# Performance work log

Hardware: AMD Instinct MI355X
Metric: run time of the kernel (lower is better)

The kernel has to match this reference:

```python
import jax, jax.numpy as jnp
import numpy as np

RATIO = 0.08  # self.ratio_3 (frozen parameter)
# kernel point k -> (dx, dy) = (k//3-1, k%3-1); matches torch.meshgrid('ij') flattening in offset_modulation
GX = np.repeat(np.arange(-1, 2), 3)  # [-1,-1,-1,0,0,0,1,1,1]
GY = np.tile(np.arange(-1, 2), 3)    # [-1,0,1,-1,0,1,-1,0,1]


def conv3(x, w, b):
    y = jax.lax.conv_general_dilated(x, w, (1, 1), ((1, 1), (1, 1)),
                                     dimension_numbers=('NCHW', 'OIHW', 'NCHW'))
    return y + b[None, :, None, None]


def offset_modulation(offset):
    B, C, H, W = offset.shape
    ov = offset.reshape(B, C // 2, 2, H, W)
    crop = ov[:, 3:12]                      # 9 (x,y) pairs
    oxy = jnp.concatenate([crop[:, :, 0], crop[:, :, 1]], axis=1) * RATIO  # [B,18,H,W]
    grid = jnp.concatenate([jnp.asarray(GX), jnp.asarray(GY)]).astype(offset.dtype)
    return oxy - grid[None, :, None, None]


def bilinear_sample(x, py, px):
    # x: [B,C,H,W]; py,px: [B,H,W] float sample coords; zero outside bounds
    B, C, H, W = x.shape
    y0 = jnp.floor(py); x0 = jnp.floor(px)
    wy = py - y0; wx = px - x0
    def gather(yi, xi):
        valid = ((yi >= 0) & (yi < H) & (xi >= 0) & (xi < W)).astype(x.dtype)
        yc = jnp.clip(yi, 0, H - 1).astype(jnp.int32)
        xc = jnp.clip(xi, 0, W - 1).astype(jnp.int32)
        g = jax.vmap(lambda img, yy, xx: img[:, yy, xx])(x, yc, xc)  # [B,C,H,W]
        return g * valid[:, None]
    return (gather(y0, x0) * ((1 - wy) * (1 - wx))[:, None]
            + gather(y0, x0 + 1) * ((1 - wy) * wx)[:, None]
            + gather(y0 + 1, x0) * (wy * (1 - wx))[:, None]
            + gather(y0 + 1, x0 + 1) * (wy * wx)[:, None])


def deform_conv(x, off, w, b):
    # off: [B,18,H,W], channels 0..8 = dx per kernel point, 9..17 = dy
    B, C, H, W = x.shape
    by = jnp.arange(H, dtype=x.dtype)[None, :, None]
    bx = jnp.arange(W, dtype=x.dtype)[None, None, :]
    out = jnp.zeros((B, w.shape[0], H, W), x.dtype)
    for k in range(9):
        py = by + GY[k] + off[:, 9 + k]
        px = bx + GX[k] + off[:, k]
        s = bilinear_sample(x, py, px)
        out = out + jnp.einsum('bchw,oc->bohw', s, w[:, :, GY[k] + 1, GX[k] + 1])
    return out + b[None, :, None, None]


def setup_inputs():
    key = jax.random.key(0)
    ks = iter(jax.random.split(key, 32))
    def p(*shape):
        return jax.random.normal(next(ks), shape, jnp.float32) * 0.05
    inp = {
        'x': jax.random.normal(next(ks), (2, 64, 256, 256), jnp.float32),
        'offset_0': jax.random.normal(next(ks), (2, 24, 256, 256), jnp.float32),
        'l12_w': p(64, 64, 3, 3), 'l12_b': p(64),
        'l13_w1': p(64, 64, 3, 3), 'l13_b1': p(64),
        'l13_w2': p(64, 64, 3, 3), 'l13_b2': p(64),
        'l14_w1': p(64, 64, 3, 3), 'l14_b1': p(64),
        'l14_w2': p(64, 64, 3, 3), 'l14_b2': p(64),
        'l15_w': p(32, 64, 3, 3), 'l15_b': p(32),
        'd50_w': p(32, 32, 3, 3), 'd50_b': p(32),
        'd51_w': p(32, 32, 3, 3), 'd51_b': p(32),
        'd60_w': p(32, 32, 3, 3), 'd60_b': p(32),
        'd61_w': p(32, 32, 3, 3), 'd61_b': p(32),
        'l24_w': p(3, 32, 3, 3), 'l24_b': p(3),
    }
    return inp


def reference(x, offset_0, l12_w, l12_b, l13_w1, l13_b1, l13_w2, l13_b2,
              l14_w1, l14_b1, l14_w2, l14_b2, l15_w, l15_b,
              d50_w, d50_b, d51_w, d51_b, d60_w, d60_b, d61_w, d61_b,
              l24_w, l24_b):
    off = offset_modulation(offset_0)
    x = conv3(x, l12_w, l12_b)
    x = conv3(jax.nn.relu(conv3(x, l13_w1, l13_b1)), l13_w2, l13_b2) + x
    x = conv3(jax.nn.relu(conv3(x, l14_w1, l14_b1)), l14_w2, l14_b2) + x
    x = conv3(x, l15_w, l15_b)
    r5 = jax.nn.relu(deform_conv(x, off, d50_w, d50_b))
    r5 = deform_conv(r5, off, d51_w, d51_b)
    x = x + r5
    r6 = jax.nn.relu(deform_conv(x, off, d60_w, d60_b))
    r6 = deform_conv(r6, off, d61_w, d61_b)
    x = x + r6
    return conv3(x, l24_w, l24_b)
```

## Files before the change

### kernel.cpp

```cpp
#include <hip/hip_runtime.h>

#define HH 256
#define WW 256
#define HW (HH * WW)

typedef float f32x4 __attribute__((ext_vector_type(4)));
typedef float f32x2 __attribute__((ext_vector_type(2)));
typedef short bf16x8 __attribute__((ext_vector_type(8)));

__device__ __forceinline__ unsigned short f2bf(float f) {
    union { float f; unsigned u; } v; v.f = f;
    unsigned r = v.u + 0x7fff + ((v.u >> 16) & 1);
    return (unsigned short)(r >> 16);
}
__device__ __forceinline__ float bflo(unsigned u) {
    union { unsigned u; float f; } v; v.u = u << 16; return v.f;
}
__device__ __forceinline__ float bfhi(unsigned u) {
    union { unsigned u; float f; } v; v.u = u & 0xffff0000u; return v.f;
}
__device__ __forceinline__ unsigned cvtpk(float lo, float hi) {
    unsigned r;
    asm("v_cvt_pk_bf16_f32 %0, %1, %2" : "=v"(r) : "v"(lo), "v"(hi));
    return r;
}
__device__ __forceinline__ f32x2 pkmul(f32x2 a, f32x2 b) {
    f32x2 d;
    asm("v_pk_mul_f32 %0, %1, %2" : "=v"(d) : "v"(a), "v"(b));
    return d;
}
__device__ __forceinline__ f32x2 pkfma(f32x2 a, f32x2 b, f32x2 c) {
    f32x2 d;
    asm("v_pk_fma_f32 %0, %1, %2, %3" : "=v"(d) : "v"(a), "v"(b), "v"(c));
    return d;
}
__device__ __forceinline__ f32x2 up2(unsigned u) {
    f32x2 r;
    union { unsigned u; float f; } lo, hi;
    lo.u = u << 16; hi.u = u & 0xffff0000u;
    r[0] = lo.f; r[1] = hi.f;
    return r;
}

template <int W>
__device__ __forceinline__ bf16x8 lerp8(const unsigned short* __restrict__ tile,
                                        int lp, float wx, float wy, int kg) {
    const unsigned short* p = tile + lp * 40 + kg * 8;
    uint4 a00 = *(const uint4*)p;
    uint4 a01 = *(const uint4*)(p + 40);
    uint4 a10 = *(const uint4*)(p + W * 40);
    uint4 a11 = *(const uint4*)(p + W * 40 + 40);
    float omx = 1.f - wx, omy = 1.f - wy;
    float s00 = omy * omx, s01 = omy * wx, s10 = wy * omx, s11 = wy * wx;
    f32x2 w00p = {s00, s00}, w01p = {s01, s01}, w10p = {s10, s10}, w11p = {s11, s11};
    unsigned c00[4] = {a00.x, a00.y, a00.z, a00.w};
    unsigned c01[4] = {a01.x, a01.y, a01.z, a01.w};
    unsigned c10[4] = {a10.x, a10.y, a10.z, a10.w};
    unsigned c11[4] = {a11.x, a11.y, a11.z, a11.w};
    union { bf16x8 v; unsigned u[4]; } ur;
#pragma unroll
    for (int j = 0; j < 4; ++j) {
        f32x2 s = pkmul(w00p, up2(c00[j]));
        s = pkfma(w01p, up2(c01[j]), s);
        s = pkfma(w10p, up2(c10[j]), s);
        s = pkfma(w11p, up2(c11[j]), s);
        ur.u[j] = cvtpk(s[0], s[1]);
    }
    return ur.v;
}

__global__ void prepack_all(
    const float* w0, const float* w1, const float* w2, const float* w3,
    const float* w4, const float* w5, const float* w6, const float* w7,
    const float* w8, const float* w9,
    unsigned short* d0, unsigned short* d1, unsigned short* d2,
    unsigned short* d3, unsigned short* d4, unsigned short* d5,
    unsigned short* d6, unsigned short* d7, unsigned short* d8,
    unsigned short* d9) {
    const int L = blockIdx.y;
    const float* w; unsigned short* dst; int COUT, CIN;
    switch (L) {
        case 0: w = w0; dst = d0; COUT = 64; CIN = 64; break;
        case 1: w = w1; dst = d1; COUT = 64; CIN = 64; break;
        case 2: w = w2; dst = d2; COUT = 64; CIN = 64; break;
        case 3: w = w3; dst = d3; COUT = 64; CIN = 64; break;
        case 4: w = w4; dst = d4; COUT = 64; CIN = 64; break;
        case 5: w = w5; dst = d5; COUT = 32; CIN = 64; break;
        case 6: w = w6; dst = d6; COUT = 32; CIN = 32; break;
        case 7: w = w7; dst = d7; COUT = 32; CIN = 32; break;
        case 8: w = w8; dst = d8; COUT = 32; CIN = 32; break;
        default: w = w9; dst = d9; COUT = 32; CIN = 32; break;
    }
    int n = COUT * CIN * 9;
    int i = blockIdx.x * 256 + threadIdx.x;
    if (i >= n) return;
    int q = i & 31;
    int rest = i >> 5;
    int o = rest % COUT;
    int rest2 = rest / COUT;
    int KC = CIN >> 5;
    int kc = rest2 % KC;
    int t = rest2 / KC;
    int cin = kc * 32 + q;
    float v = w[((o * CIN + cin) * 3 + t / 3) * 3 + (t % 3)];
    dst[i] = f2bf(v);
}

template <bool SRCF32, int CIN, int COUT, bool RELU, bool ADDRES>
__global__ __launch_bounds__((COUT / 32) * 128) void convmfma(
    const void* __restrict__ in_, const unsigned short* __restrict__ wp,
    const float* __restrict__ bias, const unsigned short* __restrict__ res,
    unsigned short* __restrict__ out) {
    constexpr int KC = CIN / 32;
    constexpr int WM = COUT / 32;
    constexpr int NT = WM * 128;
    constexpr int CSTR = (CIN == 64) ? 72 : 40;
    __shared__ unsigned short xt[204 * CSTR];

    const int tid = threadIdx.x;
    const int b = blockIdx.z;
    const int bx0 = blockIdx.x * 32;
    const int by0 = blockIdx.y * 4;

    if (SRCF32) {
        const float* inb = (const float*)in_ + (size_t)b * CIN * HW;
        for (int hp = tid; hp < 204; hp += NT) {
            int hy = hp / 34, hx = hp - hy * 34;
            int gy = by0 + hy - 1, gx = bx0 + hx - 1;
            bool ok = ((unsigned)gy < HH) && ((unsigned)gx < WW);
            const float* src = inb + ((size_t)gy * WW + gx);
            unsigned* dstp = (unsigned*)&xt[hp * CSTR];
#pragma unroll 4
            for (int c = 0; c < CIN; c += 2) {
                float v0 = ok ? src[(size_t)c * HW] : 0.f;
                float v1 = ok ? src[(size_t)(c + 1) * HW] : 0.f;
                dstp[c >> 1] = cvtpk(v0, v1);
            }
        }
    } else {
        const unsigned short* inb = (const unsigned short*)in_ + (size_t)b * HW * CIN;
        constexpr int CH = CIN / 8;
        for (int idx = tid; idx < 204 * CH; idx += NT) {
            int hp = idx / CH, sub = idx - hp * CH;
            int hy = hp / 34, hx = hp - hy * 34;
            int gy = by0 + hy - 1, gx = bx0 + hx - 1;
            uint4 v = {0, 0, 0, 0};
            if (((unsigned)gy < HH) && ((unsigned)gx < WW))
                v = *(const uint4*)&inb[((size_t)gy * WW + gx) * CIN + sub * 8];
            *(uint4*)&xt[hp * CSTR + sub * 8] = v;
        }
    }
    __syncthreads();

    const int lane = tid & 63;
    const int wv = tid >> 6;
    const int wm = (WM == 2) ? (wv & 1) : 0;
    const int wn = (WM == 2) ? (wv >> 1) : wv;
    const int l15 = lane & 15;
    const int kg = lane >> 4;

    f32x4 acc[2][4];
#pragma unroll
    for (int m = 0; m < 2; ++m)
#pragma unroll
        for (int n = 0; n < 4; ++n) acc[m][n] = {0.f, 0.f, 0.f, 0.f};

    int hbase[4];
#pragma unroll
    for (int n = 0; n < 4; ++n) {
        int p = wn * 64 + n * 16 + l15;
        hbase[n] = (p >> 5) * 34 + (p & 31);
    }

    const unsigned short* wlane = wp + ((size_t)(wm * 32 + l15) * 4 + kg) * 8;

#pragma unroll
    for (int t = 0; t < 9; ++t) {
        bf16x8 afr[2][KC];
#pragma unroll
        for (int kc = 0; kc < KC; ++kc)
#pragma unroll
            for (int m = 0; m < 2; ++m)
                afr[m][kc] = *(const bf16x8*)(wlane + ((size_t)(t * KC + kc) * COUT + m * 16) * 32);

        const int hoff = (t / 3) * 34 + (t % 3);
#pragma unroll
        for (int kc = 0; kc < KC; ++kc) {
            bf16x8 bfr[4];
#pragma unroll
            for (int n = 0; n < 4; ++n)
                bfr[n] = *(const bf16x8*)&xt[(hbase[n] + hoff) * CSTR + kc * 32 + kg * 8];
#pragma unroll
            for (int m = 0; m < 2; ++m)
#pragma unroll
                for (int n = 0; n < 4; ++n)
                    acc[m][n] = __builtin_amdgcn_mfma_f32_16x16x32_bf16(afr[m][kc], bfr[n], acc[m][n], 0, 0, 0);
        }
    }

    const size_t pixbase = (size_t)b * HW;
#pragma unroll
    for (int m = 0; m < 2; ++m) {
#pragma unroll
        for (int n = 0; n < 4; ++n) {
            int p = wn * 64 + n * 16 + l15;
            int gy = by0 + (p >> 5), gx = bx0 + (p & 31);
            size_t pidx = (pixbase + (size_t)gy * WW + gx) * COUT;
            int cb = wm * 32 + m * 16 + kg * 4;
            float v[4];
#pragma unroll
            for (int r = 0; r < 4; ++r) {
                v[r] = acc[m][n][r] + bias[cb + r];
                if (RELU) v[r] = fmaxf(v[r], 0.f);
            }
            if (ADDRES) {
                uint2 rr = *(const uint2*)&res[pidx + cb];
                v[0] += bflo(rr.x); v[1] += bfhi(rr.x);
                v[2] += bflo(rr.y); v[3] += bfhi(rr.y);
            }
            uint2 o;
            o.x = cvtpk(v[0], v[1]);
            o.y = cvtpk(v[2], v[3]);
            *(uint2*)&out[pidx + cb] = o;
        }
    }
}

__global__ __launch_bounds__(512) void dpair(
    const unsigned short* __restrict__ in, const float* __restrict__ off0,
    const unsigned short* __restrict__ w1p, const float* __restrict__ b1,
    const unsigned short* __restrict__ w2p, const float* __restrict__ b2,
    unsigned short* __restrict__ out) {
    constexpr int CS = 40;
    __shared__ unsigned short xt[432 * CS];

    const int tid = threadIdx.x;
    const int b = blockIdx.z;
    const int bx0 = blockIdx.x * 32;
    const int by0 = blockIdx.y * 8;

    const unsigned short* inb = in + (size_t)b * HW * 32;
    for (int idx = tid; idx < 432 * 4; idx += 512) {
        int hp = idx >> 2, sub = idx & 3;
        int hy = hp / 36, hx = hp - hy * 36;
        int gy = by0 + hy - 2, gx = bx0 + hx - 2;
        uint4 v = {0, 0, 0, 0};
        if (((unsigned)gy < HH) && ((unsigned)gx < WW))
            v = *(const uint4*)&inb[((size_t)gy * WW + gx) * 32 + sub * 8];
        *(uint4*)&xt[hp * CS + sub * 8] = v;
    }
    __syncthreads();

    const int lane = tid & 63;
    const int wv = tid >> 6;
    const int l15 = lane & 15;
    const int kg = lane >> 4;
    const float* offB = off0 + (size_t)b * 24 * HW;

    f32x4 acc1[2][3];
#pragma unroll
    for (int m = 0; m < 2; ++m)
#pragma unroll
        for (int f = 0; f < 3; ++f) acc1[m][f] = {0.f, 0.f, 0.f, 0.f};

    int fgy[3], fgx[3], foff[3];
#pragma unroll
    for (int f = 0; f < 3; ++f) {
        int id = (wv * 3 + f) * 16 + l15;
        int rid = min(id, 339);
        int iy = rid / 34, ix = rid - iy * 34;
        fgy[f] = by0 - 1 + iy;
        fgx[f] = bx0 - 1 + ix;
        int cy = min(max(fgy[f], 0), HH - 1);
        int cx = min(max(fgx[f], 0), WW - 1);
        foff[f] = cy * WW + cx;
    }
    const unsigned short* w1l = w1p + (size_t)(l15 * 32 + kg * 8);

#pragma unroll 1
    for (int t = 0; t < 9; ++t) {
        const int k = (t % 3) * 3 + t / 3;
        const float* offx = offB + (size_t)(6 + 2 * k) * HW;
        const float* offy = offB + (size_t)(7 + 2 * k) * HW;
        bf16x8 afr[2];
#pragma unroll
        for (int m = 0; m < 2; ++m)
            afr[m] = *(const bf16x8*)(w1l + (size_t)(t * 32 + m * 16) * 32);

#pragma unroll
        for (int f = 0; f < 3; ++f) {
            if ((wv * 3 + f) * 16 >= 340) continue;
            float dxv = offx[foff[f]] * 0.08f;
            float dyv = offy[foff[f]] * 0.08f;
            float pxf = (float)fgx[f] + dxv;
            float pyf = (float)fgy[f] + dyv;
            float x0f = floorf(pxf), y0f = floorf(pyf);
            float wx = pxf - x0f, wy = pyf - y0f;
            int tx0 = min(max((int)x0f - (bx0 - 2), 0), 34);
            int ty0 = min(max((int)y0f - (by0 - 2), 0), 10);
            bf16x8 bfr = lerp8<36>(xt, ty0 * 36 + tx0, wx, wy, kg);
#pragma unroll
            for (int m = 0; m < 2; ++m)
                acc1[m][f] = __builtin_amdgcn_mfma_f32_16x16x32_bf16(afr[m], bfr, acc1[m][f], 0, 0, 0);
        }
    }
    __syncthreads();

#pragma unroll
    for (int f = 0; f < 3; ++f) {
        int id = (wv * 3 + f) * 16 + l15;
        bool ok = ((unsigned)fgy[f] < HH) && ((unsigned)fgx[f] < WW) && (id < 340);
        int wid = min(id, 351);
#pragma unroll
        for (int m = 0; m < 2; ++m) {
            int cb = m * 16 + kg * 4;
            float v[4];
#pragma unroll
            for (int r = 0; r < 4; ++r)
                v[r] = ok ? fmaxf(acc1[m][f][r] + b1[cb + r], 0.f) : 0.f;
            uint2 o;
            o.x = cvtpk(v[0], v[1]);
            o.y = cvtpk(v[2], v[3]);
            *(uint2*)&xt[wid * CS + cb] = o;
        }
    }
    __syncthreads();

    f32x4 acc2[2][2];
#pragma unroll
    for (int m = 0; m < 2; ++m)
#pragma unroll
        for (int n = 0; n < 2; ++n) acc2[m][n] = {0.f, 0.f, 0.f, 0.f};

    const int py = by0 + wv;
    const unsigned short* w2l = w2p + (size_t)(l15 * 32 + kg * 8);

#pragma unroll 1
    for (int t = 0; t < 9; ++t) {
        const int k = (t % 3) * 3 + t / 3;
        const float* offx = offB + (size_t)(6 + 2 * k) * HW + (size_t)py * WW;
        const float* offy = offB + (size_t)(7 + 2 * k) * HW + (size_t)py * WW;
        bf16x8 afr[2];
#pragma unroll
        for (int m = 0; m < 2; ++m)
            afr[m] = *(const bf16x8*)(w2l + (size_t)(t * 32 + m * 16) * 32);

        bf16x8 bfr[2];
#pragma unroll
        for (int n = 0; n < 2; ++n) {
            const int pxi = bx0 + n * 16 + l15;
            float dxv = offx[pxi] * 0.08f;
            float dyv = offy[pxi] * 0.08f;
            float pxf = (float)pxi + dxv;
            float pyf = (float)py + dyv;
            float x0f = floorf(pxf), y0f = floorf(pyf);
            float wx = pxf - x0f, wy = pyf - y0f;
            int mx0 = min(max((int)x0f - (bx0 - 1), 0), 32);
            int my0 = min(max((int)y0f - (by0 - 1), 0), 8);
            bfr[n] = lerp8<34>(xt, my0 * 34 + mx0, wx, wy, kg);
        }
#pragma unroll
        for (int m = 0; m < 2; ++m)
#pragma unroll
            for (int n = 0; n < 2; ++n)
                acc2[m][n] = __builtin_amdgcn_mfma_f32_16x16x32_bf16(afr[m], bfr[n], acc2[m][n], 0, 0, 0);
    }

    unsigned short* outb = out + (size_t)b * HW * 32;
#pragma unroll
    for (int n = 0; n < 2; ++n) {
        int gx = bx0 + n * 16 + l15;
        size_t pidx = ((size_t)py * WW + gx) * 32;
#pragma unroll
        for (int m = 0; m < 2; ++m) {
            int cb = m * 16 + kg * 4;
            float v[4];
#pragma unroll
            for (int r = 0; r < 4; ++r) v[r] = acc2[m][n][r] + b2[cb + r];
            uint2 rr = *(const uint2*)&inb[pidx + cb];
            v[0] += bflo(rr.x); v[1] += bfhi(rr.x);
            v[2] += bflo(rr.y); v[3] += bfhi(rr.y);
            uint2 o;
            o.x = cvtpk(v[0], v[1]);
            o.y = cvtpk(v[2], v[3]);
            *(uint2*)&outb[pidx + cb] = o;
        }
    }
}

__global__ __launch_bounds__(256) void conv3f(const unsigned short* __restrict__ in,
                                              const float* __restrict__ wgt,
                                              const float* __restrict__ bias,
                                              float* __restrict__ out) {
    __shared__ unsigned short xt[324 * 34];
    const int tid = threadIdx.x;
    const int lx = tid & 15, ly = tid >> 4;
    const int bx = blockIdx.x << 4, by = blockIdx.y << 4;
    const int b = blockIdx.z;

    const unsigned short* inb = in + (size_t)b * HW * 32;
    for (int idx = tid; idx < 324 * 8; idx += 256) {
        int hp = idx >> 3, sub = idx & 7;
        int hy = hp / 18, hx = hp - hy * 18;
        int gy = by + hy - 1, gx = bx + hx - 1;
        uint2 v = {0, 0};
        if (((unsigned)gy < HH) && ((unsigned)gx < WW))
            v = *(const uint2*)&inb[((size_t)gy * WW + gx) * 32 + sub * 4];
        *(uint2*)&xt[hp * 34 + sub * 4] = v;
    }
    __syncthreads();

    float a0 = bias[0], a1 = bias[1], a2 = bias[2];
#pragma unroll
    for (int ty = 0; ty < 3; ++ty) {
#pragma unroll
        for (int tx = 0; tx < 3; ++tx) {
            const unsigned short* row = &xt[((ly + ty) * 18 + lx + tx) * 34];
#pragma unroll 8
            for (int c = 0; c < 32; c += 2) {
                unsigned pv = *(const unsigned*)&row[c];
                float vl = bflo(pv), vh = bfhi(pv);
                const float* wl = wgt + (size_t)(c * 3 + ty) * 3 + tx;
                const float* whp = wgt + (size_t)((c + 1) * 3 + ty) * 3 + tx;
                a0 = fmaf(vl, wl[0], a0);          a0 = fmaf(vh, whp[0], a0);
                a1 = fmaf(vl, wl[32 * 9], a1);     a1 = fmaf(vh, whp[32 * 9], a1);
                a2 = fmaf(vl, wl[64 * 9], a2);     a2 = fmaf(vh, whp[64 * 9], a2);
            }
        }
    }
    const size_t o0 = ((size_t)b * 3) * HW + (size_t)(by + ly) * WW + bx + lx;
    out[o0] = a0;
    out[o0 + HW] = a1;
    out[o0 + 2 * HW] = a2;
}

extern "C" void kernel_launch(void* const* d_in, const int* in_sizes, int n_in,
                              void* d_out, int out_size, void* d_ws, size_t ws_size,
                              hipStream_t stream) {
    const float* x    = (const float*)d_in[0];
    const float* off0 = (const float*)d_in[1];
    const float* w12  = (const float*)d_in[2];
    const float* b12  = (const float*)d_in[3];
    const float* w13a = (const float*)d_in[4];
    const float* b13a = (const float*)d_in[5];
    const float* w13b = (const float*)d_in[6];
    const float* b13b = (const float*)d_in[7];
    const float* w14a = (const float*)d_in[8];
    const float* b14a = (const float*)d_in[9];
    const float* w14b = (const float*)d_in[10];
    const float* b14b = (const float*)d_in[11];
    const float* w15  = (const float*)d_in[12];
    const float* b15  = (const float*)d_in[13];
    const float* w50  = (const float*)d_in[14];
    const float* b50  = (const float*)d_in[15];
    const float* w51  = (const float*)d_in[16];
    const float* b51  = (const float*)d_in[17];
    const float* w60  = (const float*)d_in[18];
    const float* b60  = (const float*)d_in[19];
    const float* w61  = (const float*)d_in[20];
    const float* b61  = (const float*)d_in[21];
    const float* w24  = (const float*)d_in[22];
    const float* b24  = (const float*)d_in[23];

    unsigned short* A  = (unsigned short*)d_ws;
    unsigned short* Bb = A + (size_t)2 * HW * 64;
    unsigned short* D  = Bb;
    unsigned short* E  = Bb + (size_t)2 * HW * 32;
    unsigned short* wpk = Bb + (size_t)2 * HW * 64;
    const int SZ64 = 64 * 64 * 9;
    const int SZ32 = 32 * 64 * 9;
    const int SZD  = 32 * 32 * 9;
    unsigned short* p12  = wpk;
    unsigned short* p13a = p12 + SZ64;
    unsigned short* p13b = p13a + SZ64;
    unsigned short* p14a = p13b + SZ64;
    unsigned short* p14b = p14a + SZ64;
    unsigned short* p15  = p14b + SZ64;
    unsigned short* q50  = p15 + SZ32;
    unsigned short* q51  = q50 + SZD;
    unsigned short* q60  = q51 + SZD;
    unsigned short* q61  = q60 + SZD;
    float* out = (float*)d_out;

    prepack_all<<<dim3(144, 10), 256, 0, stream>>>(
        w12, w13a, w13b, w14a, w14b, w15, w50, w51, w60, w61,
        p12, p13a, p13b, p14a, p14b, p15, q50, q51, q60, q61);

    dim3 gm(WW / 32, HH / 4, 2);
    dim3 gd(WW / 32, HH / 8, 2);
    dim3 gs(HH / 16, WW / 16, 2);

    convmfma<true,  64, 64, false, false><<<gm, 256, 0, stream>>>(x,  p12,  b12,  nullptr, A);
    convmfma<false, 64, 64, true,  false><<<gm, 256, 0, stream>>>(A,  p13a, b13a, nullptr, Bb);
    convmfma<false, 64, 64, false, true ><<<gm, 256, 0, stream>>>(Bb, p13b, b13b, A, A);
    convmfma<false, 64, 64, true,  false><<<gm, 256, 0, stream>>>(A,  p14a, b14a, nullptr, Bb);
    convmfma<false, 64, 64, false, true ><<<gm, 256, 0, stream>>>(Bb, p14b, b14b, A, A);
    convmfma<false, 64, 32, false, false><<<gm, 128, 0, stream>>>(A,  p15,  b15,  nullptr, D);

    dpair<<<gd, 512, 0, stream>>>(D, off0, q50, b50, q51, b51, E);
    dpair<<<gd, 512, 0, stream>>>(E, off0, q60, b60, q61, b61, D);
    conv3f<<<gs, 256, 0, stream>>>(D, w24, b24, out);
}
```

Baseline: 221.0 us.

## Prefetch deform offsets one tap ahead and split mid-tile LDS buffer

In the fused deform-conv pair kernel, the per-tap offset loads are software-pipelined: the offsets for the next kernel tap are loaded into registers while the current tap's bilinear gather and MFMAs run, which hides global-memory latency. The intermediate (relu of the first conv) tile now goes to a separate LDS region instead of overwriting the input tile, so one __syncthreads between the two stages is removed. The cost is more LDS per block (784 instead of 432 rows of 40 bf16, about 62 KB), which may lower occupancy, and extra registers for the prefetched values.

```diff
diff --git a/kernel.cpp b/kernel.cpp
--- a/kernel.cpp
+++ b/kernel.cpp
@@ -232,7 +232,8 @@
     const unsigned short* __restrict__ w2p, const float* __restrict__ b2,
     unsigned short* __restrict__ out) {
     constexpr int CS = 40;
-    __shared__ unsigned short xt[432 * CS];
+    constexpr int MIDB = 432 * CS;
+    __shared__ unsigned short xt[(432 + 352) * CS];
 
     const int tid = threadIdx.x;
     const int b = blockIdx.z;
@@ -277,11 +278,23 @@
     }
     const unsigned short* w1l = w1p + (size_t)(l15 * 32 + kg * 8);
 
+    float cdx[3], cdy[3];
+#pragma unroll
+    for (int f = 0; f < 3; ++f) {
+        cdx[f] = offB[(size_t)6 * HW + foff[f]];
+        cdy[f] = offB[(size_t)7 * HW + foff[f]];
+    }
+
 #pragma unroll 1
     for (int t = 0; t < 9; ++t) {
-        const int k = (t % 3) * 3 + t / 3;
-        const float* offx = offB + (size_t)(6 + 2 * k) * HW;
-        const float* offy = offB + (size_t)(7 + 2 * k) * HW;
+        float ndx[3], ndy[3];
+        if (t < 8) {
+            const int kn = ((t + 1) % 3) * 3 + (t + 1) / 3;
+            const float* nx = offB + (size_t)(6 + 2 * kn) * HW;
+            const float* ny = offB + (size_t)(7 + 2 * kn) * HW;
+#pragma unroll
+            for (int f = 0; f < 3; ++f) { ndx[f] = nx[foff[f]]; ndy[f] = ny[foff[f]]; }
+        }
         bf16x8 afr[2];
 #pragma unroll
         for (int m = 0; m < 2; ++m)
@@ -290,8 +303,8 @@
 #pragma unroll
         for (int f = 0; f < 3; ++f) {
             if ((wv * 3 + f) * 16 >= 340) continue;
-            float dxv = offx[foff[f]] * 0.08f;
-            float dyv = offy[foff[f]] * 0.08f;
+            float dxv = cdx[f] * 0.08f;
+            float dyv = cdy[f] * 0.08f;
             float pxf = (float)fgx[f] + dxv;
             float pyf = (float)fgy[f] + dyv;
             float x0f = floorf(pxf), y0f = floorf(pyf);
@@ -303,8 +316,11 @@
             for (int m = 0; m < 2; ++m)
                 acc1[m][f] = __builtin_amdgcn_mfma_f32_16x16x32_bf16(afr[m], bfr, acc1[m][f], 0, 0, 0);
         }
-    }
-    __syncthreads();
+        if (t < 8) {
+#pragma unroll
+            for (int f = 0; f < 3; ++f) { cdx[f] = ndx[f]; cdy[f] = ndy[f]; }
+        }
+    }
 
 #pragma unroll
     for (int f = 0; f < 3; ++f) {
@@ -321,7 +337,7 @@
             uint2 o;
             o.x = cvtpk(v[0], v[1]);
             o.y = cvtpk(v[2], v[3]);
-            *(uint2*)&xt[wid * CS + cb] = o;
+            *(uint2*)&xt[MIDB + wid * CS + cb] = o;
         }
     }
     __syncthreads();
@@ -334,12 +350,26 @@
 
     const int py = by0 + wv;
     const unsigned short* w2l = w2p + (size_t)(l15 * 32 + kg * 8);
+    const int prow = py * WW;
+    const int pxi[2] = {bx0 + l15, bx0 + 16 + l15};
+
+    float cdx2[2], cdy2[2];
+#pragma unroll
+    for (int n = 0; n < 2; ++n) {
+        cdx2[n] = offB[(size_t)6 * HW + prow + pxi[n]];
+        cdy2[n] = offB[(size_t)7 * HW + prow + pxi[n]];
+    }
 
 #pragma unroll 1
     for (int t = 0; t < 9; ++t) {
-        const int k = (t % 3) * 3 + t / 3;
-        const float* offx = offB + (size_t)(6 + 2 * k) * HW + (size_t)py * WW;
-        const float* offy = offB + (size_t)(7 + 2 * k) * HW + (size_t)py * WW;
+        float ndx[2], ndy[2];
+        if (t < 8) {
+            const int kn = ((t + 1) % 3) * 3 + (t + 1) / 3;
+            const float* nx = offB + (size_t)(6 + 2 * kn) * HW + prow;
+            const float* ny = offB + (size_t)(7 + 2 * kn) * HW + prow;
+#pragma unroll
+            for (int n = 0; n < 2; ++n) { ndx[n] = nx[pxi[n]]; ndy[n] = ny[pxi[n]]; }
+        }
         bf16x8 afr[2];
 #pragma unroll
         for (int m = 0; m < 2; ++m)
@@ -348,29 +378,31 @@
         bf16x8 bfr[2];
 #pragma unroll
         for (int n = 0; n < 2; ++n) {
-            const int pxi = bx0 + n * 16 + l15;
-            float dxv = offx[pxi] * 0.08f;
-            float dyv = offy[pxi] * 0.08f;
-            float pxf = (float)pxi + dxv;
+            float dxv = cdx2[n] * 0.08f;
+            float dyv = cdy2[n] * 0.08f;
+            float pxf = (float)pxi[n] + dxv;
             float pyf = (float)py + dyv;
             float x0f = floorf(pxf), y0f = floorf(pyf);
             float wx = pxf - x0f, wy = pyf - y0f;
             int mx0 = min(max((int)x0f - (bx0 - 1), 0), 32);
             int my0 = min(max((int)y0f - (by0 - 1), 0), 8);
-            bfr[n] = lerp8<34>(xt, my0 * 34 + mx0, wx, wy, kg);
+            bfr[n] = lerp8<34>(xt + MIDB, my0 * 34 + mx0, wx, wy, kg);
         }
 #pragma unroll
         for (int m = 0; m < 2; ++m)
 #pragma unroll
             for (int n = 0; n < 2; ++n)
                 acc2[m][n] = __builtin_amdgcn_mfma_f32_16x16x32_bf16(afr[m], bfr[n], acc2[m][n], 0, 0, 0);
+        if (t < 8) {
+#pragma unroll
+            for (int n = 0; n < 2; ++n) { cdx2[n] = ndx[n]; cdy2[n] = ndy[n]; }
+        }
     }
 
     unsigned short* outb = out + (size_t)b * HW * 32;
 #pragma unroll
     for (int n = 0; n < 2; ++n) {
-        int gx = bx0 + n * 16 + l15;
-        size_t pidx = ((size_t)py * WW + gx) * 32;
+        size_t pidx = ((size_t)prow + pxi[n]) * 32;
 #pragma unroll
         for (int m = 0; m < 2; ++m) {
             int cb = m * 16 + kg * 4;
```

Measured after the change: 216.9 us, median of 3. Within noise of the previous version (-1.9%).
